# Kernel optimization log

Measured on AMD Instinct MI355X. Metric: run time of the kernel, lower is better.

Reference implementation:

```python
import jax, jax.numpy as jnp
from jax import lax
import numpy as np

# Mamba mixer dims (mamba-1.4b scale)
D_MODEL, D_INNER, D_STATE, D_CONV, DT_RANK = 2048, 4096, 16, 4, 128
B, L = 2, 1024


def setup_inputs() -> dict:
    key = jax.random.key(0)
    ks = jax.random.split(key, 10)
    s = 0.02
    x = jax.random.normal(ks[0], (B, L, D_MODEL), jnp.float32)
    W_in = jax.random.normal(ks[1], (2 * D_INNER, D_MODEL), jnp.float32) * s
    conv_w = jax.random.normal(ks[2], (D_INNER, D_CONV), jnp.float32) * s  # depthwise kernel
    conv_b = jax.random.normal(ks[3], (D_INNER,), jnp.float32) * s
    W_x = jax.random.normal(ks[4], (DT_RANK + 2 * D_STATE, D_INNER), jnp.float32) * s
    W_dt = jax.random.normal(ks[5], (D_INNER, DT_RANK), jnp.float32) * s
    b_dt = jax.random.normal(ks[6], (D_INNER,), jnp.float32) * s
    # S4D-real init: A = -[1..d_state] per channel
    A_log = jnp.log(jnp.broadcast_to(jnp.arange(1, D_STATE + 1, dtype=jnp.float32), (D_INNER, D_STATE)))
    Dp = jnp.ones((D_INNER,), jnp.float32)
    W_out = jax.random.normal(ks[7], (D_MODEL, D_INNER), jnp.float32) * s
    return {"x": x, "W_in": W_in, "conv_w": conv_w, "conv_b": conv_b,
            "W_x": W_x, "W_dt": W_dt, "b_dt": b_dt, "A_log": A_log,
            "Dp": Dp, "W_out": W_out}


def reference(x, W_in, conv_w, conv_b, W_x, W_dt, b_dt, A_log, Dp, W_out):
    b, l, _ = x.shape
    d_inner, d_state = A_log.shape
    dt_rank = W_dt.shape[1]
    d_conv = conv_w.shape[1]

    # in_proj -> x branch and gate z   [b,l,2*d_inner]
    xz = jnp.einsum('bld,ed->ble', x, W_in)
    xp, z = jnp.split(xz, 2, axis=-1)

    # causal depthwise conv1d (kernel size d_conv) + SiLU
    xpad = jnp.pad(xp, ((0, 0), (d_conv - 1, 0), (0, 0)))
    xc = conv_b + sum(xpad[:, k:k + l, :] * conv_w[:, k] for k in range(d_conv))
    xc = jax.nn.silu(xc)

    # input-dependent dt, B, C
    dbc = jnp.einsum('ble,fe->blf', xc, W_x)
    dt = dbc[..., :dt_rank]
    Bm = dbc[..., dt_rank:dt_rank + d_state]          # [b,l,s]
    Cm = dbc[..., dt_rank + d_state:]                 # [b,l,s]
    delta = jax.nn.softplus(jnp.einsum('blr,er->ble', dt, W_dt) + b_dt)  # [b,l,e]

    A = -jnp.exp(A_log)                               # [e,s]
    dA = jnp.exp(delta[..., None] * A)                # [b,l,e,s]
    dBx = delta[..., None] * Bm[:, :, None, :] * xc[..., None]  # [b,l,e,s]

    def step(h, inp):
        dA_t, dBx_t = inp                             # [b,e,s]
        h = dA_t * h + dBx_t
        return h, h

    h0 = jnp.zeros((b, d_inner, d_state), x.dtype)
    _, hs = lax.scan(step, h0, (jnp.swapaxes(dA, 0, 1), jnp.swapaxes(dBx, 0, 1)))
    hs = jnp.swapaxes(hs, 0, 1)                       # [b,l,e,s]

    y = jnp.einsum('bles,bls->ble', hs, Cm) + xc * Dp
    y = y * jax.nn.silu(z)
    return jnp.einsum('ble,de->bld', y, W_out)
```

## Files before the change

kernel.cpp:

```cpp
#include <hip/hip_runtime.h>
#include <cstdint>


typedef __bf16 bf16x8 __attribute__((ext_vector_type(8)));
typedef float f32x4 __attribute__((ext_vector_type(4)));

__device__ __forceinline__ unsigned short f2bf(float f) {
  uint32_t u = __float_as_uint(f);
  u += 0x7FFFu + ((u >> 16) & 1u);
  return (unsigned short)(u >> 16);
}

__device__ __forceinline__ float bf2f(unsigned short v) {
  return __uint_as_float(((uint32_t)v) << 16);
}

__device__ __forceinline__ float silu_f(float v) {
  return v / (1.f + __expf(-v));
}

__device__ __forceinline__ float softplus_f(float v) {
  return (v > 20.f) ? v : log1pf(__expf(v));
}

__global__ void cast_all(const float* __restrict__ x, const float* __restrict__ W_in,
                         const float* __restrict__ W_out, const float* __restrict__ W_dt,
                         const float* __restrict__ W_x,
                         unsigned short* __restrict__ x_bf, unsigned short* __restrict__ Win_bf,
                         unsigned short* __restrict__ Wout_bf, unsigned short* __restrict__ Wdt_bf,
                         unsigned short* __restrict__ Wx_bf) {
  int i = blockIdx.x * 256 + threadIdx.x;
  const float4* s4; ushort4* d4; int j;
  if (i < 1048576)      { s4 = (const float4*)x;     d4 = (ushort4*)x_bf;    j = i; }
  else if (i < 5242880) { s4 = (const float4*)W_in;  d4 = (ushort4*)Win_bf;  j = i - 1048576; }
  else if (i < 7340032) { s4 = (const float4*)W_out; d4 = (ushort4*)Wout_bf; j = i - 5242880; }
  else if (i < 7471104) { s4 = (const float4*)W_dt;  d4 = (ushort4*)Wdt_bf;  j = i - 7340032; }
  else {
    j = i - 7471104;
    ushort4 o = {0, 0, 0, 0};
    if (j < 163840) {
      float4 v = ((const float4*)W_x)[j];
      o.x = f2bf(v.x); o.y = f2bf(v.y); o.z = f2bf(v.z); o.w = f2bf(v.w);
    }
    ((ushort4*)Wx_bf)[j] = o;
    return;
  }
  float4 v = s4[j];
  ushort4 o; o.x = f2bf(v.x); o.y = f2bf(v.y); o.z = f2bf(v.z); o.w = f2bf(v.w);
  d4[j] = o;
}

#define BM 128
#define BN 128
#define BKK 32

__device__ __forceinline__ void stage_tile(const unsigned short* __restrict__ G,
                                           int ldK, int g0, int k0,
                                           unsigned short* lds, int wave, int lane) {
#pragma unroll
  for (int c = 0; c < 2; ++c) {
    int row = c * 64 + wave * 16 + (lane >> 2);
    int col = (lane & 3) * 8;
    const unsigned short* src = G + (size_t)(g0 + row) * ldK + (k0 + col);
    unsigned short* dst = lds + c * 2048 + wave * 512;
    __builtin_amdgcn_global_load_lds((__attribute__((address_space(1))) void*)(src),
                                     (__attribute__((address_space(3))) void*)(dst),
                                     16, 0, 0);
  }
}

__global__ __launch_bounds__(256)
void gemm_bt(const unsigned short* __restrict__ A, const unsigned short* __restrict__ B,
             float* __restrict__ C, int M, int N, int ldK, int kchunk,
             const float* __restrict__ bias_sp) {
  __shared__ unsigned short As[BM * BKK];
  __shared__ unsigned short Bs[BN * BKK];
  const int tid = threadIdx.x;
  const int wave = tid >> 6, lane = tid & 63;
  const int wr = wave >> 1, wc = wave & 1;
  const int m0 = blockIdx.y * BM, n0 = blockIdx.x * BN;
  const int lr = lane & 15, lg = lane >> 4;
  const int kb = blockIdx.z * kchunk, ke = kb + kchunk;
  C += (size_t)blockIdx.z * M * N;

  f32x4 zero = {0.f, 0.f, 0.f, 0.f};
  f32x4 acc[4][4];
#pragma unroll
  for (int i = 0; i < 4; ++i)
#pragma unroll
    for (int j = 0; j < 4; ++j) acc[i][j] = zero;

  for (int k0 = kb; k0 < ke; k0 += BKK) {
    stage_tile(A, ldK, m0, k0, As, wave, lane);
    stage_tile(B, ldK, n0, k0, Bs, wave, lane);
    __syncthreads();
    bf16x8 af[4], bfr[4];
#pragma unroll
    for (int i = 0; i < 4; ++i)
      af[i] = *reinterpret_cast<const bf16x8*>(&As[(wr * 64 + i * 16 + lr) * BKK + lg * 8]);
#pragma unroll
    for (int j = 0; j < 4; ++j)
      bfr[j] = *reinterpret_cast<const bf16x8*>(&Bs[(wc * 64 + j * 16 + lr) * BKK + lg * 8]);
#pragma unroll
    for (int i = 0; i < 4; ++i)
#pragma unroll
      for (int j = 0; j < 4; ++j)
        acc[i][j] = __builtin_amdgcn_mfma_f32_16x16x32_bf16(af[i], bfr[j], acc[i][j], 0, 0, 0);
    __syncthreads();
  }

#pragma unroll
  for (int i = 0; i < 4; ++i) {
#pragma unroll
    for (int j = 0; j < 4; ++j) {
      int mrow = m0 + wr * 64 + i * 16 + lg * 4;
      int ncol = n0 + wc * 64 + j * 16 + lr;
      if (bias_sp) {
        float bv = bias_sp[ncol];
#pragma unroll
        for (int r = 0; r < 4; ++r)
          C[(size_t)(mrow + r) * N + ncol] = softplus_f(acc[i][j][r] + bv);
      } else {
#pragma unroll
        for (int r = 0; r < 4; ++r)
          C[(size_t)(mrow + r) * N + ncol] = acc[i][j][r];
      }
    }
  }
}

__global__ void reduce8_dbc(const float* __restrict__ p, float* __restrict__ dbc,
                            unsigned short* __restrict__ dt_bf) {
  int i = blockIdx.x * 256 + threadIdx.x;
  float s = 0.f;
#pragma unroll
  for (int c = 0; c < 8; ++c) s += p[(size_t)c * 524288 + i];
  dbc[i] = s;
  int col = i & 255;
  if (col < 128) dt_bf[(size_t)(i >> 8) * 128 + col] = f2bf(s);
}

__global__ void reduce4_out(const float* __restrict__ p, float* __restrict__ out) {
  int i = blockIdx.x * 256 + threadIdx.x;
  const float4* p4 = reinterpret_cast<const float4*>(p);
  float4 a = p4[i], b = p4[i + 1048576], c = p4[i + 2097152], d = p4[i + 3145728];
  float4 r;
  r.x = (a.x + b.x) + (c.x + d.x); r.y = (a.y + b.y) + (c.y + d.y);
  r.z = (a.z + b.z) + (c.z + d.z); r.w = (a.w + b.w) + (c.w + d.w);
  reinterpret_cast<float4*>(out)[i] = r;
}

template <typename OT>
__global__ __launch_bounds__(512, 2)
void gemm_bt_8ph(const unsigned short* __restrict__ A,
                 const unsigned short* __restrict__ B,
                 OT* __restrict__ C, int M, int N, int K, int nbm, int kchunk) {
  __shared__ unsigned short As[2][16384];
  __shared__ unsigned short Bs[2][16384];
  const int tid = threadIdx.x;
  const int wid = tid >> 6, lane = tid & 63;
  const int wr = wid >> 2, wc = wid & 3;
  const int lr = lane & 15, lg = lane >> 4;

  const int cpx = gridDim.x >> 3;
  const int x = blockIdx.x;
  const int wg = (x & 7) * cpx + (x >> 3);
  const int bm = wg % nbm, bn = wg / nbm;
  const int m0 = bm * 256, n0 = bn * 256;
  const int kb = blockIdx.z * kchunk;
  C += (size_t)blockIdx.z * M * N;

  f32x4 acc[8][4];
  f32x4 zero = {0.f, 0.f, 0.f, 0.f};
#pragma unroll
  for (int i = 0; i < 8; ++i)
#pragma unroll
    for (int j = 0; j < 4; ++j) acc[i][j] = zero;

  const int nt = kchunk / 64;

  auto QUANT = [&](int t, int q) {
    const int buf = t & 1;
    const int ks = q >> 1;
    const unsigned short* G = (q & 1) ? B : A;
    const int g0 = (q & 1) ? n0 : m0;
    unsigned short* lds = ((q & 1) ? &Bs[buf][0] : &As[buf][0]) + ks * 8192;
    const int k0 = kb + t * 64 + ks * 32;
#pragma unroll
    for (int r = 0; r < 2; ++r) {
      int row = r * 128 + (tid >> 2);
      int scol = ((tid & 3) * 8) ^ (((row >> 1) & 3) << 3);
      const unsigned short* src = G + (size_t)(g0 + row) * K + (k0 + scol);
      __builtin_amdgcn_global_load_lds(
          (__attribute__((address_space(1))) const void*)(src),
          (__attribute__((address_space(3))) void*)(lds + r * 4096 + tid * 8),
          16, 0, 0);
    }
  };

  auto RD_A = [&](int buf, int ks, int mf) -> bf16x8 {
    int row = wr * 128 + mf * 16 + lr;
    int col = (lg * 8) ^ (((row >> 1) & 3) << 3);
    return *reinterpret_cast<const bf16x8*>(&As[buf][ks * 8192 + row * 32 + col]);
  };
  auto RD_B = [&](int buf, int ks, int nf) -> bf16x8 {
    int row = wc * 64 + nf * 16 + lr;
    int col = (lg * 8) ^ (((row >> 1) & 3) << 3);
    return *reinterpret_cast<const bf16x8*>(&Bs[buf][ks * 8192 + row * 32 + col]);
  };

  QUANT(0, 0); QUANT(0, 1); QUANT(0, 2); QUANT(0, 3);
  asm volatile("s_waitcnt vmcnt(4)" ::: "memory");
  __builtin_amdgcn_s_barrier();

  bf16x8 a[8], b[4];
  for (int t = 0; t < nt; ++t) {
    const int buf = t & 1;
    const bool pf = (t + 1 < nt);
#pragma unroll
    for (int mf = 0; mf < 8; ++mf) a[mf] = RD_A(buf, 0, mf);
    b[0] = RD_B(buf, 0, 0); b[1] = RD_B(buf, 0, 1);
    if (pf) {
      QUANT(t + 1, 0);
      asm volatile("s_waitcnt vmcnt(6)" ::: "memory");
    } else {
      asm volatile("s_waitcnt vmcnt(4)" ::: "memory");
    }
    __builtin_amdgcn_s_barrier();
    asm volatile("s_waitcnt lgkmcnt(0)" ::: "memory");
    __builtin_amdgcn_sched_barrier(0);
    __builtin_amdgcn_s_setprio(1);
#pragma unroll
    for (int nf = 0; nf < 2; ++nf)
#pragma unroll
      for (int mf = 0; mf < 8; ++mf)
        acc[mf][nf] = __builtin_amdgcn_mfma_f32_16x16x32_bf16(a[mf], b[nf], acc[mf][nf], 0, 0, 0);
    __builtin_amdgcn_s_setprio(0);
    __builtin_amdgcn_s_barrier();
    b[2] = RD_B(buf, 0, 2); b[3] = RD_B(buf, 0, 3);
    if (pf) {
      QUANT(t + 1, 1);
      asm volatile("s_waitcnt vmcnt(4)" ::: "memory");
    } else {
      asm volatile("s_waitcnt vmcnt(0)" ::: "memory");
    }
    __builtin_amdgcn_s_barrier();
    asm volatile("s_waitcnt lgkmcnt(0)" ::: "memory");
    __builtin_amdgcn_sched_barrier(0);
    __builtin_amdgcn_s_setprio(1);
#pragma unroll
    for (int nf = 2; nf < 4; ++nf)
#pragma unroll
      for (int mf = 0; mf < 8; ++mf)
        acc[mf][nf] = __builtin_amdgcn_mfma_f32_16x16x32_bf16(a[mf], b[nf], acc[mf][nf], 0, 0, 0);
    __builtin_amdgcn_s_setprio(0);
    __builtin_amdgcn_s_barrier();
#pragma unroll
    for (int mf = 0; mf < 8; ++mf) a[mf] = RD_A(buf, 1, mf);
    b[0] = RD_B(buf, 1, 0); b[1] = RD_B(buf, 1, 1);
    if (pf) QUANT(t + 1, 2);
    __builtin_amdgcn_s_barrier();
    asm volatile("s_waitcnt lgkmcnt(0)" ::: "memory");
    __builtin_amdgcn_sched_barrier(0);
    __builtin_amdgcn_s_setprio(1);
#pragma unroll
    for (int nf = 0; nf < 2; ++nf)
#pragma unroll
      for (int mf = 0; mf < 8; ++mf)
        acc[mf][nf] = __builtin_amdgcn_mfma_f32_16x16x32_bf16(a[mf], b[nf], acc[mf][nf], 0, 0, 0);
    __builtin_amdgcn_s_setprio(0);
    __builtin_amdgcn_s_barrier();
    b[2] = RD_B(buf, 1, 2); b[3] = RD_B(buf, 1, 3);
    if (pf) {
      QUANT(t + 1, 3);
      asm volatile("s_waitcnt vmcnt(4)" ::: "memory");
    }
    __builtin_amdgcn_s_barrier();
    asm volatile("s_waitcnt lgkmcnt(0)" ::: "memory");
    __builtin_amdgcn_sched_barrier(0);
    __builtin_amdgcn_s_setprio(1);
#pragma unroll
    for (int nf = 2; nf < 4; ++nf)
#pragma unroll
      for (int mf = 0; mf < 8; ++mf)
        acc[mf][nf] = __builtin_amdgcn_mfma_f32_16x16x32_bf16(a[mf], b[nf], acc[mf][nf], 0, 0, 0);
    __builtin_amdgcn_s_setprio(0);
    __builtin_amdgcn_s_barrier();
  }

#pragma unroll
  for (int mf = 0; mf < 8; ++mf) {
#pragma unroll
    for (int nf = 0; nf < 4; ++nf) {
      int mrow = m0 + wr * 128 + mf * 16 + lg * 4;
      int ncol = n0 + wc * 64 + nf * 16 + lr;
#pragma unroll
      for (int r = 0; r < 4; ++r) {
        if constexpr (sizeof(OT) == 2)
          C[(size_t)(mrow + r) * N + ncol] = (OT)f2bf(acc[mf][nf][r]);
        else
          C[(size_t)(mrow + r) * N + ncol] = (OT)acc[mf][nf][r];
      }
    }
  }
}

__global__ void conv_silu_kernel(const unsigned short* __restrict__ xzb,
                                 const float* __restrict__ conv_w,
                                 const float* __restrict__ conv_b,
                                 unsigned short* __restrict__ xc_bf) {
  int i4 = blockIdx.x * 256 + threadIdx.x;
  int e4 = i4 & 1023;
  int m = i4 >> 10;
  int l = m & 1023;
  float4 cw0 = reinterpret_cast<const float4*>(conv_w)[e4 * 4 + 0];
  float4 cw1 = reinterpret_cast<const float4*>(conv_w)[e4 * 4 + 1];
  float4 cw2 = reinterpret_cast<const float4*>(conv_w)[e4 * 4 + 2];
  float4 cw3 = reinterpret_cast<const float4*>(conv_w)[e4 * 4 + 3];
  float4 acc = reinterpret_cast<const float4*>(conv_b)[e4];
#pragma unroll
  for (int k = 0; k < 4; ++k) {
    if (l - 3 + k >= 0) {
      ushort4 xv = reinterpret_cast<const ushort4*>(xzb)[(size_t)(m - 3 + k) * 2048 + e4];
      acc.x = fmaf(bf2f(xv.x), ((const float*)&cw0)[k], acc.x);
      acc.y = fmaf(bf2f(xv.y), ((const float*)&cw1)[k], acc.y);
      acc.z = fmaf(bf2f(xv.z), ((const float*)&cw2)[k], acc.z);
      acc.w = fmaf(bf2f(xv.w), ((const float*)&cw3)[k], acc.w);
    }
  }
  ushort4 o;
  o.x = f2bf(silu_f(acc.x)); o.y = f2bf(silu_f(acc.y));
  o.z = f2bf(silu_f(acc.z)); o.w = f2bf(silu_f(acc.w));
  reinterpret_cast<ushort4*>(xc_bf)[i4] = o;
}

__device__ __forceinline__ void dA_powers(float r, float* dA) {
  float r2 = r * r, r4 = r2 * r2, r8 = r4 * r4;
  dA[0] = r;        dA[1] = r2;       dA[2] = r2 * r;   dA[3] = r4;
  dA[4] = r4 * r;   dA[5] = r4 * r2;  dA[6] = dA[5] * r; dA[7] = r8;
  dA[8] = r8 * r;   dA[9] = r8 * r2;  dA[10] = dA[9] * r; dA[11] = r8 * r4;
  dA[12] = dA[11] * r; dA[13] = dA[11] * r2; dA[14] = dA[13] * r; dA[15] = r8 * r8;
}

__global__ __launch_bounds__(256)
void scan_pass1(const float* __restrict__ delta, const float* __restrict__ dbc,
                const unsigned short* __restrict__ xcb, const float* __restrict__ A_log,
                float* __restrict__ hfin, float* __restrict__ Pprod) {
  __shared__ float Bsh[1024];
  const int tid = threadIdx.x;
  const int bc = blockIdx.x >> 4;
  const int eg = blockIdx.x & 15;
  const int b = bc >> 4, c = bc & 15;
  const int e = eg * 256 + tid;
  const int mb = b * 1024 + c * 64;
  for (int i = tid; i < 1024; i += 256)
    Bsh[i] = dbc[(size_t)(mb + (i >> 4)) * 256 + 128 + (i & 15)];
  __syncthreads();

  float A[16];
  const float4* al = reinterpret_cast<const float4*>(A_log + (size_t)e * 16);
#pragma unroll
  for (int q = 0; q < 4; ++q) {
    float4 v = al[q];
    A[q * 4 + 0] = -__expf(v.x); A[q * 4 + 1] = -__expf(v.y);
    A[q * 4 + 2] = -__expf(v.z); A[q * 4 + 3] = -__expf(v.w);
  }
  bool fastp = true;
#pragma unroll
  for (int s = 0; s < 16; ++s)
    fastp = fastp && (fabsf(A[s] + (float)(s + 1)) <= 1e-5f * (float)(s + 1));

  float h[16], P[16];
#pragma unroll
  for (int s = 0; s < 16; ++s) { h[s] = 0.f; P[s] = 1.f; }

  if (fastp) {
    for (int ll = 0; ll < 64; ++ll) {
      const size_t m = (size_t)(mb + ll);
      float dl = delta[m * 4096 + e];
      float dxc = dl * bf2f(xcb[m * 4096 + e]);
      float dA[16];
      dA_powers(__expf(-dl), dA);
#pragma unroll
      for (int s = 0; s < 16; ++s) {
        P[s] *= dA[s];
        h[s] = fmaf(dA[s], h[s], Bsh[ll * 16 + s] * dxc);
      }
    }
  } else {
    for (int ll = 0; ll < 64; ++ll) {
      const size_t m = (size_t)(mb + ll);
      float dl = delta[m * 4096 + e];
      float dxc = dl * bf2f(xcb[m * 4096 + e]);
#pragma unroll
      for (int s = 0; s < 16; ++s) {
        float dA = __expf(dl * A[s]);
        P[s] *= dA;
        h[s] = fmaf(dA, h[s], Bsh[ll * 16 + s] * dxc);
      }
    }
  }
  float* hp = hfin + ((size_t)bc * 4096 + e) * 16;
  float* pp = Pprod + ((size_t)bc * 4096 + e) * 16;
#pragma unroll
  for (int s = 0; s < 16; ++s) { hp[s] = h[s]; pp[s] = P[s]; }
}

__global__ void scan_pass2(float* __restrict__ hfin, const float* __restrict__ Pprod) {
  int idx = blockIdx.x * 256 + threadIdx.x;
  int b = idx >> 16;
  int es = idx & 65535;
  float H = 0.f;
  for (int c = 0; c < 16; ++c) {
    size_t o = ((size_t)(b * 16 + c) << 16) + es;
    float hf = hfin[o];
    float Pp = Pprod[o];
    hfin[o] = H;
    H = fmaf(Pp, H, hf);
  }
}

__global__ __launch_bounds__(256)
void scan_pass3(const float* __restrict__ delta, const float* __restrict__ dbc,
                const unsigned short* __restrict__ xcb, const unsigned short* __restrict__ xzb,
                const float* __restrict__ A_log, const float* __restrict__ Dp,
                const float* __restrict__ hcarry, unsigned short* __restrict__ y_bf) {
  __shared__ float Bsh[1024];
  __shared__ float Csh[1024];
  const int tid = threadIdx.x;
  const int bc = blockIdx.x >> 4;
  const int eg = blockIdx.x & 15;
  const int b = bc >> 4, c = bc & 15;
  const int e = eg * 256 + tid;
  const int mb = b * 1024 + c * 64;
  for (int i = tid; i < 1024; i += 256) {
    size_t base = (size_t)(mb + (i >> 4)) * 256 + (i & 15);
    Bsh[i] = dbc[base + 128];
    Csh[i] = dbc[base + 144];
  }
  __syncthreads();

  float A[16];
  const float4* al = reinterpret_cast<const float4*>(A_log + (size_t)e * 16);
#pragma unroll
  for (int q = 0; q < 4; ++q) {
    float4 v = al[q];
    A[q * 4 + 0] = -__expf(v.x); A[q * 4 + 1] = -__expf(v.y);
    A[q * 4 + 2] = -__expf(v.z); A[q * 4 + 3] = -__expf(v.w);
  }
  bool fastp = true;
#pragma unroll
  for (int s = 0; s < 16; ++s)
    fastp = fastp && (fabsf(A[s] + (float)(s + 1)) <= 1e-5f * (float)(s + 1));

  float h[16];
  const float* hp = hcarry + ((size_t)bc * 4096 + e) * 16;
#pragma unroll
  for (int s = 0; s < 16; ++s) h[s] = hp[s];
  const float Dv = Dp[e];

  if (fastp) {
    for (int ll = 0; ll < 64; ++ll) {
      const size_t m = (size_t)(mb + ll);
      float dl = delta[m * 4096 + e];
      float xcv = bf2f(xcb[m * 4096 + e]);
      float dxc = dl * xcv;
      float dA[16];
      dA_powers(__expf(-dl), dA);
      float y = 0.f;
#pragma unroll
      for (int s = 0; s < 16; ++s) {
        h[s] = fmaf(dA[s], h[s], Bsh[ll * 16 + s] * dxc);
        y = fmaf(h[s], Csh[ll * 16 + s], y);
      }
      float z = bf2f(xzb[m * 8192 + 4096 + e]);
      y = (y + xcv * Dv) * silu_f(z);
      y_bf[m * 4096 + e] = f2bf(y);
    }
  } else {
    for (int ll = 0; ll < 64; ++ll) {
      const size_t m = (size_t)(mb + ll);
      float dl = delta[m * 4096 + e];
      float xcv = bf2f(xcb[m * 4096 + e]);
      float dxc = dl * xcv;
      float y = 0.f;
#pragma unroll
      for (int s = 0; s < 16; ++s) {
        float dA = __expf(dl * A[s]);
        h[s] = fmaf(dA, h[s], Bsh[ll * 16 + s] * dxc);
        y = fmaf(h[s], Csh[ll * 16 + s], y);
      }
      float z = bf2f(xzb[m * 8192 + 4096 + e]);
      y = (y + xcv * Dv) * silu_f(z);
      y_bf[m * 4096 + e] = f2bf(y);
    }
  }
}

extern "C" void kernel_launch(void* const* d_in, const int* in_sizes, int n_in,
                              void* d_out, int out_size, void* d_ws, size_t ws_size,
                              hipStream_t stream) {
  const float* x      = (const float*)d_in[0];
  const float* W_in   = (const float*)d_in[1];
  const float* conv_w = (const float*)d_in[2];
  const float* conv_b = (const float*)d_in[3];
  const float* W_x    = (const float*)d_in[4];
  const float* W_dt   = (const float*)d_in[5];
  const float* b_dt   = (const float*)d_in[6];
  const float* A_log  = (const float*)d_in[7];
  const float* Dp     = (const float*)d_in[8];
  const float* W_out  = (const float*)d_in[9];
  float* out = (float*)d_out;
  char* ws = (char*)d_ws;

  unsigned short* Win_bf    = (unsigned short*)(ws + 0);
  float*          gpart2    = (float*)(ws + 0);
  float*          delta     = (float*)(ws + 0);
  unsigned short* x_bf      = (unsigned short*)(ws + 33554432);
  unsigned short* y_bf      = (unsigned short*)(ws + 33554432);
  unsigned short* Wout_bf   = (unsigned short*)(ws + 50331648);
  unsigned short* Wx_bf     = (unsigned short*)(ws + 67108864);
  unsigned short* Wdt_bf    = (unsigned short*)(ws + 69206016);
  unsigned short* xz_bf     = (unsigned short*)(ws + 70254592);
  float*          gpart4    = (float*)(ws + 103809024);
  float*          hfin      = (float*)(ws + 103809024);
  float*          Pprod     = (float*)(ws + 112197632);
  unsigned short* xc_bf     = (unsigned short*)(ws + 170917888);
  float*          dbc       = (float*)(ws + 187695104);
  unsigned short* dt_bf     = (unsigned short*)(ws + 189792256);

  cast_all<<<30208, 256, 0, stream>>>(x, W_in, W_out, W_dt, W_x,
                                      x_bf, Win_bf, Wout_bf, Wdt_bf, Wx_bf);

  gemm_bt_8ph<unsigned short><<<256, 512, 0, stream>>>(x_bf, Win_bf, xz_bf, 2048, 8192, 2048, 8, 2048);

  conv_silu_kernel<<<8192, 256, 0, stream>>>(xz_bf, conv_w, conv_b, xc_bf);

  gemm_bt<<<dim3(2, 16, 8), 256, 0, stream>>>(xc_bf, Wx_bf, gpart2, 2048, 256, 4096, 512, nullptr);
  reduce8_dbc<<<2048, 256, 0, stream>>>(gpart2, dbc, dt_bf);

  gemm_bt<<<dim3(32, 16, 1), 256, 0, stream>>>(dt_bf, Wdt_bf, delta, 2048, 4096, 128, 128, b_dt);

  scan_pass1<<<512, 256, 0, stream>>>(delta, dbc, xc_bf, A_log, hfin, Pprod);
  scan_pass2<<<512, 256, 0, stream>>>(hfin, Pprod);
  scan_pass3<<<512, 256, 0, stream>>>(delta, dbc, xc_bf, xz_bf, A_log, Dp, hfin, y_bf);

  gemm_bt_8ph<float><<<dim3(64, 1, 4), 512, 0, stream>>>(y_bf, Wout_bf, gpart4, 2048, 2048, 4096, 8, 1024);
  reduce4_out<<<4096, 256, 0, stream>>>(gpart4, out);
}
```

Baseline: 330.1 us.

## Split GEMM A-fragment loads into halves and compute scan chunk decay from summed delta

The GEMM main loop now holds 4 A fragments instead of 8 and loads all 4 B fragments per phase, splitting each k-step into two M-halves. This reduces register pressure and changes where global prefetch (QUANT) calls and vmcnt waits fall. In the scan's fast path, the running product of per-step decays is replaced by exp(-sum(delta)) raised to powers once at the end, removing 16 multiplies per step. The cost is reordered LDS reads with different overlap, and a small rounding difference in the decay product.

```diff
diff --git a/kernel.cpp b/kernel.cpp
--- a/kernel.cpp
+++ b/kernel.cpp
@@ -213,34 +213,31 @@
   asm volatile("s_waitcnt vmcnt(4)" ::: "memory");
   __builtin_amdgcn_s_barrier();
 
-  bf16x8 a[8], b[4];
+  bf16x8 a[4], b[4];
   for (int t = 0; t < nt; ++t) {
     const int buf = t & 1;
     const bool pf = (t + 1 < nt);
 #pragma unroll
-    for (int mf = 0; mf < 8; ++mf) a[mf] = RD_A(buf, 0, mf);
-    b[0] = RD_B(buf, 0, 0); b[1] = RD_B(buf, 0, 1);
-    if (pf) {
-      QUANT(t + 1, 0);
-      asm volatile("s_waitcnt vmcnt(6)" ::: "memory");
-    } else {
-      asm volatile("s_waitcnt vmcnt(4)" ::: "memory");
-    }
+    for (int mf = 0; mf < 4; ++mf) a[mf] = RD_A(buf, 0, mf);
+#pragma unroll
+    for (int nf = 0; nf < 4; ++nf) b[nf] = RD_B(buf, 0, nf);
+    if (pf) { QUANT(t + 1, 0); QUANT(t + 1, 1); }
     __builtin_amdgcn_s_barrier();
     asm volatile("s_waitcnt lgkmcnt(0)" ::: "memory");
     __builtin_amdgcn_sched_barrier(0);
     __builtin_amdgcn_s_setprio(1);
 #pragma unroll
-    for (int nf = 0; nf < 2; ++nf)
-#pragma unroll
-      for (int mf = 0; mf < 8; ++mf)
+    for (int nf = 0; nf < 4; ++nf)
+#pragma unroll
+      for (int mf = 0; mf < 4; ++mf)
         acc[mf][nf] = __builtin_amdgcn_mfma_f32_16x16x32_bf16(a[mf], b[nf], acc[mf][nf], 0, 0, 0);
     __builtin_amdgcn_s_setprio(0);
     __builtin_amdgcn_s_barrier();
-    b[2] = RD_B(buf, 0, 2); b[3] = RD_B(buf, 0, 3);
+#pragma unroll
+    for (int mf = 0; mf < 4; ++mf) a[mf] = RD_A(buf, 0, mf + 4);
     if (pf) {
-      QUANT(t + 1, 1);
-      asm volatile("s_waitcnt vmcnt(4)" ::: "memory");
+      QUANT(t + 1, 2);
+      asm volatile("s_waitcnt vmcnt(6)" ::: "memory");
     } else {
       asm volatile("s_waitcnt vmcnt(0)" ::: "memory");
     }
@@ -249,41 +246,40 @@
     __builtin_amdgcn_sched_barrier(0);
     __builtin_amdgcn_s_setprio(1);
 #pragma unroll
-    for (int nf = 2; nf < 4; ++nf)
-#pragma unroll
-      for (int mf = 0; mf < 8; ++mf)
-        acc[mf][nf] = __builtin_amdgcn_mfma_f32_16x16x32_bf16(a[mf], b[nf], acc[mf][nf], 0, 0, 0);
+    for (int nf = 0; nf < 4; ++nf)
+#pragma unroll
+      for (int mf = 0; mf < 4; ++mf)
+        acc[mf + 4][nf] = __builtin_amdgcn_mfma_f32_16x16x32_bf16(a[mf], b[nf], acc[mf + 4][nf], 0, 0, 0);
     __builtin_amdgcn_s_setprio(0);
     __builtin_amdgcn_s_barrier();
 #pragma unroll
-    for (int mf = 0; mf < 8; ++mf) a[mf] = RD_A(buf, 1, mf);
-    b[0] = RD_B(buf, 1, 0); b[1] = RD_B(buf, 1, 1);
-    if (pf) QUANT(t + 1, 2);
+    for (int mf = 0; mf < 4; ++mf) a[mf] = RD_A(buf, 1, mf);
+#pragma unroll
+    for (int nf = 0; nf < 4; ++nf) b[nf] = RD_B(buf, 1, nf);
+    if (pf) QUANT(t + 1, 3);
     __builtin_amdgcn_s_barrier();
     asm volatile("s_waitcnt lgkmcnt(0)" ::: "memory");
     __builtin_amdgcn_sched_barrier(0);
     __builtin_amdgcn_s_setprio(1);
 #pragma unroll
-    for (int nf = 0; nf < 2; ++nf)
-#pragma unroll
-      for (int mf = 0; mf < 8; ++mf)
+    for (int nf = 0; nf < 4; ++nf)
+#pragma unroll
+      for (int mf = 0; mf < 4; ++mf)
         acc[mf][nf] = __builtin_amdgcn_mfma_f32_16x16x32_bf16(a[mf], b[nf], acc[mf][nf], 0, 0, 0);
     __builtin_amdgcn_s_setprio(0);
     __builtin_amdgcn_s_barrier();
-    b[2] = RD_B(buf, 1, 2); b[3] = RD_B(buf, 1, 3);
-    if (pf) {
-      QUANT(t + 1, 3);
-      asm volatile("s_waitcnt vmcnt(4)" ::: "memory");
-    }
+#pragma unroll
+    for (int mf = 0; mf < 4; ++mf) a[mf] = RD_A(buf, 1, mf + 4);
+    if (pf) asm volatile("s_waitcnt vmcnt(4)" ::: "memory");
     __builtin_amdgcn_s_barrier();
     asm volatile("s_waitcnt lgkmcnt(0)" ::: "memory");
     __builtin_amdgcn_sched_barrier(0);
     __builtin_amdgcn_s_setprio(1);
 #pragma unroll
-    for (int nf = 2; nf < 4; ++nf)
-#pragma unroll
-      for (int mf = 0; mf < 8; ++mf)
-        acc[mf][nf] = __builtin_amdgcn_mfma_f32_16x16x32_bf16(a[mf], b[nf], acc[mf][nf], 0, 0, 0);
+    for (int nf = 0; nf < 4; ++nf)
+#pragma unroll
+      for (int mf = 0; mf < 4; ++mf)
+        acc[mf + 4][nf] = __builtin_amdgcn_mfma_f32_16x16x32_bf16(a[mf], b[nf], acc[mf + 4][nf], 0, 0, 0);
     __builtin_amdgcn_s_setprio(0);
     __builtin_amdgcn_s_barrier();
   }
@@ -375,18 +371,19 @@
   for (int s = 0; s < 16; ++s) { h[s] = 0.f; P[s] = 1.f; }
 
   if (fastp) {
+    float sd = 0.f;
     for (int ll = 0; ll < 64; ++ll) {
       const size_t m = (size_t)(mb + ll);
       float dl = delta[m * 4096 + e];
       float dxc = dl * bf2f(xcb[m * 4096 + e]);
+      sd += dl;
       float dA[16];
       dA_powers(__expf(-dl), dA);
 #pragma unroll
-      for (int s = 0; s < 16; ++s) {
-        P[s] *= dA[s];
+      for (int s = 0; s < 16; ++s)
         h[s] = fmaf(dA[s], h[s], Bsh[ll * 16 + s] * dxc);
-      }
-    }
+    }
+    dA_powers(__expf(-sd), P);
   } else {
     for (int ll = 0; ll < 64; ++ll) {
       const size_t m = (size_t)(mb + ll);
```

Result: no change. 331.8 us (+0.5%).
